# Kernel tuning notes

Measured on AMD Instinct MI355X. Metric: run time of the kernel, lower is better.

## Reference

```python
import jax, jax.numpy as jnp
import numpy as np

EPSILON = 0.15
N_ITERS = 20

def _l2_normalize(x, eps=1e-12):
    n = jnp.linalg.norm(x, axis=-1, keepdims=True)
    return x / jnp.maximum(n, eps)

def setup_inputs() -> dict:
    key = jax.random.key(0)
    k1, k2, k3 = jax.random.split(key, 3)
    B, Ta, Tv, D = 16, 2048, 1024, 512
    return {
        "audio": jax.random.normal(k1, (B, Ta, D), dtype=jnp.float32),
        "video": jax.random.normal(k2, (B, Tv, D), dtype=jnp.float32),
        "quality": jax.random.uniform(k3, (B, Tv), dtype=jnp.float32),
        "lambda_time": jnp.float32(0.5),
        "lambda_qual": jnp.float32(5.0),
    }

def reference(audio, video, quality, lambda_time, lambda_qual):
    B, Ta, D = audio.shape
    Tv = video.shape[1]
    # --- cost matrix ---
    a = _l2_normalize(audio)
    v = _l2_normalize(video)
    sim = jnp.einsum('bad,bvd->bav', a, v)  # [B,Ta,Tv]
    i = jnp.arange(Ta, dtype=jnp.float32)[:, None]
    j = jnp.arange(Tv, dtype=jnp.float32)[None, :]
    time_dist = jnp.abs(i / Ta - j / Tv)  # [Ta,Tv]
    cost = (1.0 - sim) + lambda_time * time_dist[None] \
           + lambda_qual * (1.0 - quality)[:, None, :]
    # --- log-space Sinkhorn (fixed n_iters) ---
    K = -cost / EPSILON
    u0 = jnp.zeros((B, Ta), dtype=cost.dtype)
    v0 = jnp.zeros((B, Tv), dtype=cost.dtype)
    def body(_, uv):
        u, vv = uv
        u = -jax.scipy.special.logsumexp(K + vv[:, None, :], axis=2)
        vv = -jax.scipy.special.logsumexp(K + u[:, :, None], axis=1)
        return (u, vv)
    u, vv = jax.lax.fori_loop(0, N_ITERS, body, (u0, v0))
    transport = jnp.exp(K + u[:, :, None] + vv[:, None, :])
    transport = transport / (jnp.sum(transport, axis=-1, keepdims=True) + 1e-8)
    return transport
```

## Files before the change

kernel.cpp:

```cpp
#include <hip/hip_runtime.h>
#include <hip/hip_fp16.h>

#define B_  16
#define TA  2048
#define TV  1024
#define DD  512
#define NIT 20

static constexpr float EPSI  = 0.15f;
static constexpr float LOG2E = 1.4426950408889634f;

using f32x4 = __attribute__((ext_vector_type(4))) float;
using half8 = __attribute__((ext_vector_type(8))) _Float16;
using half4 = __attribute__((ext_vector_type(4))) _Float16;

__device__ inline float wave_sum(float x) {
  #pragma unroll
  for (int m = 32; m; m >>= 1) x += __shfl_xor(x, m, 64);
  return x;
}

__global__ __launch_bounds__(256) void norms_k(const float* __restrict__ audio,
                                               const float* __restrict__ video,
                                               float* __restrict__ inv_na,
                                               float* __restrict__ inv_nv) {
  int wid  = (blockIdx.x * blockDim.x + threadIdx.x) >> 6;
  int lane = threadIdx.x & 63;
  const float* src;
  float* dst;
  if (wid < B_ * TA) { src = audio + (size_t)wid * DD; dst = inv_na + wid; }
  else               { src = video + (size_t)(wid - B_ * TA) * DD; dst = inv_nv + (wid - B_ * TA); }
  const float4* s4 = (const float4*)src;
  float ss = 0.f;
  #pragma unroll
  for (int i = 0; i < 2; i++) {
    float4 v = s4[lane + i * 64];
    ss += v.x * v.x + v.y * v.y + v.z * v.z + v.w * v.w;
  }
  ss = wave_sum(ss);
  if (lane == 0) *dst = 1.0f / fmaxf(sqrtf(ss), 1e-12f);
}

__global__ void vinit_k(const float* __restrict__ quality,
                        const float* __restrict__ lam_q,
                        float* __restrict__ Vp) {
  int i = blockIdx.x * blockDim.x + threadIdx.x;
  float c1 = LOG2E / EPSI;
  Vp[i] = -c1 * (*lam_q) * (1.0f - quality[i]);
}

#define BM 128
#define BN 128
#define BK 64
#define LDH 72

template<bool F16>
__global__ __launch_bounds__(256) void cost_k(const float* __restrict__ audio,
                                              const float* __restrict__ video,
                                              const float* __restrict__ inv_na,
                                              const float* __restrict__ inv_nv,
                                              const float* __restrict__ lam_t,
                                              float* __restrict__ Kb,
                                              _Float16* __restrict__ Kh) {
  __shared__ _Float16 As[BM * LDH];
  __shared__ _Float16 Bs[BN * LDH];
  int b  = blockIdx.z;
  int a0 = blockIdx.x * BM;
  int j0 = blockIdx.y * BN;
  int tid  = threadIdx.x;
  int lane = tid & 63;
  int wid  = tid >> 6;
  int wm = wid >> 1, wn = wid & 1;

  const float* Ab = audio + (size_t)b * TA * DD;
  const float* Vb = video + (size_t)b * TV * DD;

  f32x4 acc[4][4];
  #pragma unroll
  for (int i = 0; i < 4; i++)
    #pragma unroll
    for (int j = 0; j < 4; j++)
      #pragma unroll
      for (int r = 0; r < 4; r++) acc[i][j][r] = 0.f;

  int frow = tid >> 4;
  int fcol = (tid & 15) * 4;
  int l16 = lane & 15, lq = lane >> 4;

  for (int kb = 0; kb < DD; kb += BK) {
    __syncthreads();
    #pragma unroll
    for (int s = 0; s < 8; s++) {
      int r = frow + s * 16;
      float4 v = *(const float4*)&Ab[(size_t)(a0 + r) * DD + kb + fcol];
      float sc = inv_na[b * TA + a0 + r];
      half4 h = { (_Float16)(v.x * sc), (_Float16)(v.y * sc),
                  (_Float16)(v.z * sc), (_Float16)(v.w * sc) };
      *(half4*)&As[r * LDH + fcol] = h;
    }
    #pragma unroll
    for (int s = 0; s < 8; s++) {
      int r = frow + s * 16;
      float4 v = *(const float4*)&Vb[(size_t)(j0 + r) * DD + kb + fcol];
      float sc = inv_nv[b * TV + j0 + r];
      half4 h = { (_Float16)(v.x * sc), (_Float16)(v.y * sc),
                  (_Float16)(v.z * sc), (_Float16)(v.w * sc) };
      *(half4*)&Bs[r * LDH + fcol] = h;
    }
    __syncthreads();
    #pragma unroll
    for (int ks = 0; ks < 2; ks++) {
      half8 af[4], bf[4];
      #pragma unroll
      for (int mf = 0; mf < 4; mf++)
        af[mf] = *(const half8*)&As[(wm * 64 + mf * 16 + l16) * LDH + ks * 32 + lq * 8];
      #pragma unroll
      for (int nf = 0; nf < 4; nf++)
        bf[nf] = *(const half8*)&Bs[(wn * 64 + nf * 16 + l16) * LDH + ks * 32 + lq * 8];
      #pragma unroll
      for (int mf = 0; mf < 4; mf++)
        #pragma unroll
        for (int nf = 0; nf < 4; nf++)
          acc[mf][nf] = __builtin_amdgcn_mfma_f32_16x16x32_f16(af[mf], bf[nf], acc[mf][nf], 0, 0, 0);
    }
  }

  float lt = *lam_t;
  float c1 = LOG2E / EPSI;
  #pragma unroll
  for (int mf = 0; mf < 4; mf++)
    #pragma unroll
    for (int nf = 0; nf < 4; nf++)
      #pragma unroll
      for (int r = 0; r < 4; r++) {
        int a = a0 + wm * 64 + mf * 16 + lq * 4 + r;
        int j = j0 + wn * 64 + nf * 16 + l16;
        float sim = acc[mf][nf][r];
        float td = fabsf((float)a * (1.0f / TA) - (float)j * (1.0f / TV));
        float val = c1 * (sim - 1.0f - lt * td);
        size_t o = ((size_t)b * TA + a) * TV + j;
        if constexpr (F16) Kh[o] = (_Float16)val;
        else               Kb[o] = val;
      }
}

__global__ __launch_bounds__(512) void iter16_k(const _Float16* __restrict__ Kh,
                                                const float* __restrict__ Vp,
                                                float* __restrict__ pc) {
  __shared__ float lc[8][1024];
  int tid = threadIdx.x, lane = tid & 63, wid = tid >> 6;
  int row0 = (blockIdx.x * 8 + wid) * 8;
  int b = row0 >> 11;
  const float* vp = Vp + b * TV + lane * 8;
  float vpl[16];
  *(float4*)&vpl[0]  = *(const float4*)&vp[0];
  *(float4*)&vpl[4]  = *(const float4*)&vp[4];
  *(float4*)&vpl[8]  = *(const float4*)&vp[512];
  *(float4*)&vpl[12] = *(const float4*)&vp[516];
  float C[16];
  #pragma unroll
  for (int i = 0; i < 16; i++) C[i] = 0.f;

  #pragma unroll 2
  for (int r = 0; r < 8; r++) {
    const _Float16* row = Kh + (size_t)(row0 + r) * TV + lane * 8;
    half8 h0 = *(const half8*)&row[0];
    half8 h1 = *(const half8*)&row[512];
    float e[16];
    float s = 0.f;
    #pragma unroll
    for (int i = 0; i < 8; i++) { e[i] = exp2f((float)h0[i] + vpl[i]); s += e[i]; }
    #pragma unroll
    for (int i = 0; i < 8; i++) { e[8 + i] = exp2f((float)h1[i] + vpl[8 + i]); s += e[8 + i]; }
    s = wave_sum(s);
    float w = 1.0f / s;
    #pragma unroll
    for (int i = 0; i < 16; i++) C[i] = fmaf(e[i], w, C[i]);
  }

  *(float4*)&lc[wid][lane * 8]       = make_float4(C[0], C[1], C[2], C[3]);
  *(float4*)&lc[wid][lane * 8 + 4]   = make_float4(C[4], C[5], C[6], C[7]);
  *(float4*)&lc[wid][512 + lane * 8]     = make_float4(C[8], C[9], C[10], C[11]);
  *(float4*)&lc[wid][512 + lane * 8 + 4] = make_float4(C[12], C[13], C[14], C[15]);
  __syncthreads();
  #pragma unroll
  for (int k = 0; k < 2; k++) {
    int col = tid + k * 512;
    float S = 0.f;
    #pragma unroll
    for (int w = 0; w < 8; w++) S += lc[w][col];
    pc[(size_t)blockIdx.x * 1024 + col] = S;
  }
}

__global__ __launch_bounds__(512) void iter32_k(const float* __restrict__ Kb,
                                                const float* __restrict__ Vp,
                                                float* __restrict__ pc) {
  __shared__ float lc[8][1024];
  int tid = threadIdx.x, lane = tid & 63, wid = tid >> 6;
  int row0 = (blockIdx.x * 8 + wid) * 8;
  int b = row0 >> 11;
  const float* vp = Vp + b * TV;
  float vpl[16];
  #pragma unroll
  for (int q = 0; q < 4; q++)
    *(float4*)&vpl[q * 4] = *(const float4*)&vp[q * 256 + lane * 4];
  float C[16];
  #pragma unroll
  for (int i = 0; i < 16; i++) C[i] = 0.f;

  #pragma unroll 2
  for (int r = 0; r < 8; r++) {
    const float* row = Kb + (size_t)(row0 + r) * TV;
    float e[16];
    float s = 0.f;
    #pragma unroll
    for (int q = 0; q < 4; q++) {
      float4 kv = *(const float4*)&row[q * 256 + lane * 4];
      e[q*4+0] = exp2f(kv.x + vpl[q*4+0]);
      e[q*4+1] = exp2f(kv.y + vpl[q*4+1]);
      e[q*4+2] = exp2f(kv.z + vpl[q*4+2]);
      e[q*4+3] = exp2f(kv.w + vpl[q*4+3]);
      s += e[q*4+0] + e[q*4+1] + e[q*4+2] + e[q*4+3];
    }
    s = wave_sum(s);
    float w = 1.0f / s;
    #pragma unroll
    for (int i = 0; i < 16; i++) C[i] = fmaf(e[i], w, C[i]);
  }

  #pragma unroll
  for (int q = 0; q < 4; q++)
    *(float4*)&lc[wid][q * 256 + lane * 4] =
        make_float4(C[q*4+0], C[q*4+1], C[q*4+2], C[q*4+3]);
  __syncthreads();
  #pragma unroll
  for (int k = 0; k < 2; k++) {
    int col = tid + k * 512;
    float S = 0.f;
    #pragma unroll
    for (int w = 0; w < 8; w++) S += lc[w][col];
    pc[(size_t)blockIdx.x * 1024 + col] = S;
  }
}

__global__ void vcomb_k(const float* __restrict__ pc, float* __restrict__ Vp) {
  int i = blockIdx.x * blockDim.x + threadIdx.x;
  int b = i >> 10, j = i & 1023;
  const float* p = pc + (size_t)(b * 32) * 1024 + j;
  float S = 0.f;
  #pragma unroll
  for (int c = 0; c < 32; c++) S += p[c * 1024];
  Vp[i] -= log2f(S);
}

__global__ __launch_bounds__(256) void final16_k(const _Float16* __restrict__ Kh,
                                                 const float* __restrict__ Vp,
                                                 float* __restrict__ out) {
  int gw   = (blockIdx.x * blockDim.x + threadIdx.x) >> 6;
  int lane = threadIdx.x & 63;
  int b = gw >> 11;
  const float* vp = Vp + b * TV + lane * 8;
  float vpl[16];
  *(float4*)&vpl[0]  = *(const float4*)&vp[0];
  *(float4*)&vpl[4]  = *(const float4*)&vp[4];
  *(float4*)&vpl[8]  = *(const float4*)&vp[512];
  *(float4*)&vpl[12] = *(const float4*)&vp[516];
  const _Float16* row = Kh + (size_t)gw * TV + lane * 8;
  half8 h0 = *(const half8*)&row[0];
  half8 h1 = *(const half8*)&row[512];
  float e[16];
  float s = 0.f;
  #pragma unroll
  for (int i = 0; i < 8; i++) { e[i] = exp2f((float)h0[i] + vpl[i]); s += e[i]; }
  #pragma unroll
  for (int i = 0; i < 8; i++) { e[8 + i] = exp2f((float)h1[i] + vpl[8 + i]); s += e[8 + i]; }
  s = wave_sum(s);
  float inv = 1.0f / s;
  float* o = out + (size_t)gw * TV + lane * 8;
  *(float4*)&o[0]   = make_float4(e[0] * inv, e[1] * inv, e[2] * inv, e[3] * inv);
  *(float4*)&o[4]   = make_float4(e[4] * inv, e[5] * inv, e[6] * inv, e[7] * inv);
  *(float4*)&o[512] = make_float4(e[8] * inv, e[9] * inv, e[10] * inv, e[11] * inv);
  *(float4*)&o[516] = make_float4(e[12] * inv, e[13] * inv, e[14] * inv, e[15] * inv);
}

__global__ __launch_bounds__(256) void final32_k(float* __restrict__ Kb,
                                                 const float* __restrict__ Vp) {
  int gw   = (blockIdx.x * blockDim.x + threadIdx.x) >> 6;
  int lane = threadIdx.x & 63;
  int b = gw >> 11;
  const float* vp = Vp + b * TV;
  float* row = Kb + (size_t)gw * TV;
  float e[16];
  float s = 0.f;
  #pragma unroll
  for (int q = 0; q < 4; q++) {
    float4 kv = *(const float4*)&row[q * 256 + lane * 4];
    float4 vv = *(const float4*)&vp[q * 256 + lane * 4];
    e[q*4+0] = exp2f(kv.x + vv.x); e[q*4+1] = exp2f(kv.y + vv.y);
    e[q*4+2] = exp2f(kv.z + vv.z); e[q*4+3] = exp2f(kv.w + vv.w);
    s += e[q*4+0] + e[q*4+1] + e[q*4+2] + e[q*4+3];
  }
  s = wave_sum(s);
  float inv = 1.0f / s;
  #pragma unroll
  for (int q = 0; q < 4; q++)
    *(float4*)&row[q * 256 + lane * 4] =
        make_float4(e[q*4+0] * inv, e[q*4+1] * inv, e[q*4+2] * inv, e[q*4+3] * inv);
}

extern "C" void kernel_launch(void* const* d_in, const int* in_sizes, int n_in,
                              void* d_out, int out_size, void* d_ws, size_t ws_size,
                              hipStream_t stream) {
  const float* audio   = (const float*)d_in[0];
  const float* video   = (const float*)d_in[1];
  const float* quality = (const float*)d_in[2];
  const float* lam_t   = (const float*)d_in[3];
  const float* lam_q   = (const float*)d_in[4];

  float* out = (float*)d_out;
  float* ws  = (float*)d_ws;
  float* inv_na = ws;
  float* inv_nv = ws + 32768;
  float* Vp     = ws + 49152;
  float* pc     = ws + 65536;
  _Float16* Kh  = (_Float16*)(ws + 589824);

  size_t need_f16 = 589824ull * 4 + (size_t)B_ * TA * TV * 2;

  norms_k<<<12288, 256, 0, stream>>>(audio, video, inv_na, inv_nv);
  vinit_k<<<64, 256, 0, stream>>>(quality, lam_q, Vp);

  if (ws_size >= need_f16) {
    cost_k<true><<<dim3(16, 8, 16), 256, 0, stream>>>(audio, video, inv_na, inv_nv,
                                                      lam_t, nullptr, Kh);
    for (int it = 0; it < NIT; it++) {
      iter16_k<<<512, 512, 0, stream>>>(Kh, Vp, pc);
      vcomb_k<<<64, 256, 0, stream>>>(pc, Vp);
    }
    final16_k<<<8192, 256, 0, stream>>>(Kh, Vp, out);
  } else {
    float* Kb = out;
    cost_k<false><<<dim3(16, 8, 16), 256, 0, stream>>>(audio, video, inv_na, inv_nv,
                                                       lam_t, Kb, nullptr);
    for (int it = 0; it < NIT; it++) {
      iter32_k<<<512, 512, 0, stream>>>(Kb, Vp, pc);
      vcomb_k<<<64, 256, 0, stream>>>(pc, Vp);
    }
    final32_k<<<8192, 256, 0, stream>>>(Kb, Vp);
  }
}
```

Baseline: 486.1 us.

## Fuse Sinkhorn dual update into row pass, pre-normalize inputs to fp16

Adds a new path, used when the workspace is large enough. It first converts normalized audio and video to fp16 in the norms pass, so the GEMM loads half-precision tiles directly and uses a grouped block order. Each Sinkhorn step now reduces the previous step's per-block column partials and applies the log2 update at its own start, which removes the separate vcomb launch. Partials and the V vectors are double-buffered, and the final normalization is folded into the last step. This costs more workspace, redundant 32-way partial reductions in every block, and an extra fp16 copy of the inputs.

```diff
diff --git a/kernel.cpp b/kernel.cpp
--- a/kernel.cpp
+++ b/kernel.cpp
@@ -18,6 +18,38 @@
   #pragma unroll
   for (int m = 32; m; m >>= 1) x += __shfl_xor(x, m, 64);
   return x;
+}
+
+__device__ inline int swz(int c) { return c ^ (((c >> 5) & 7) << 2); }
+
+__global__ __launch_bounds__(256) void norms2_k(const float* __restrict__ audio,
+                                                const float* __restrict__ video,
+                                                _Float16* __restrict__ af16,
+                                                _Float16* __restrict__ vf16,
+                                                float* __restrict__ inv_na,
+                                                float* __restrict__ inv_nv) {
+  int wid  = (blockIdx.x * blockDim.x + threadIdx.x) >> 6;
+  int lane = threadIdx.x & 63;
+  const float* src; _Float16* dst; float* ndst;
+  if (wid < B_ * TA) {
+    src = audio + (size_t)wid * DD; dst = af16 + (size_t)wid * DD; ndst = inv_na + wid;
+  } else {
+    int w2 = wid - B_ * TA;
+    src = video + (size_t)w2 * DD; dst = vf16 + (size_t)w2 * DD; ndst = inv_nv + w2;
+  }
+  float4 v0 = ((const float4*)src)[lane];
+  float4 v1 = ((const float4*)src)[lane + 64];
+  float ss = v0.x*v0.x + v0.y*v0.y + v0.z*v0.z + v0.w*v0.w
+           + v1.x*v1.x + v1.y*v1.y + v1.z*v1.z + v1.w*v1.w;
+  ss = wave_sum(ss);
+  float sc = 1.0f / fmaxf(sqrtf(ss), 1e-12f);
+  if (lane == 0) *ndst = sc;
+  half4 h0 = { (_Float16)(v0.x * sc), (_Float16)(v0.y * sc),
+               (_Float16)(v0.z * sc), (_Float16)(v0.w * sc) };
+  half4 h1 = { (_Float16)(v1.x * sc), (_Float16)(v1.y * sc),
+               (_Float16)(v1.z * sc), (_Float16)(v1.w * sc) };
+  ((half4*)dst)[lane]      = h0;
+  ((half4*)dst)[lane + 64] = h1;
 }
 
 __global__ __launch_bounds__(256) void norms_k(const float* __restrict__ audio,
@@ -26,8 +58,7 @@
                                                float* __restrict__ inv_nv) {
   int wid  = (blockIdx.x * blockDim.x + threadIdx.x) >> 6;
   int lane = threadIdx.x & 63;
-  const float* src;
-  float* dst;
+  const float* src; float* dst;
   if (wid < B_ * TA) { src = audio + (size_t)wid * DD; dst = inv_na + wid; }
   else               { src = video + (size_t)(wid - B_ * TA) * DD; dst = inv_nv + (wid - B_ * TA); }
   const float4* s4 = (const float4*)src;
@@ -53,6 +84,193 @@
 #define BN 128
 #define BK 64
 #define LDH 72
+
+__global__ __launch_bounds__(256) void cost2_k(const _Float16* __restrict__ af16,
+                                               const _Float16* __restrict__ vf16,
+                                               const float* __restrict__ lam_t,
+                                               _Float16* __restrict__ Kh) {
+  __shared__ _Float16 As[BM * LDH];
+  __shared__ _Float16 Bs[BN * LDH];
+  int lin = blockIdx.x;
+  int sw  = (lin & 7) * 256 + (lin >> 3);
+  int b   = sw >> 7;
+  int rem = sw & 127;
+  int j0  = (rem >> 4) * BN;
+  int a0  = (rem & 15) * BM;
+  int tid  = threadIdx.x;
+  int lane = tid & 63;
+  int wid  = tid >> 6;
+  int wm = wid >> 1, wn = wid & 1;
+
+  const _Float16* Ab = af16 + (size_t)b * TA * DD;
+  const _Float16* Vb = vf16 + (size_t)b * TV * DD;
+
+  f32x4 acc[4][4];
+  #pragma unroll
+  for (int i = 0; i < 4; i++)
+    #pragma unroll
+    for (int j = 0; j < 4; j++)
+      #pragma unroll
+      for (int r = 0; r < 4; r++) acc[i][j][r] = 0.f;
+
+  int srow = tid >> 3;
+  int sc8  = (tid & 7) * 8;
+  int l16 = lane & 15, lq = lane >> 4;
+
+  for (int kb = 0; kb < DD; kb += BK) {
+    __syncthreads();
+    #pragma unroll
+    for (int s = 0; s < 4; s++) {
+      int r = srow + s * 32;
+      *(half8*)&As[r * LDH + sc8] = *(const half8*)&Ab[(size_t)(a0 + r) * DD + kb + sc8];
+      *(half8*)&Bs[r * LDH + sc8] = *(const half8*)&Vb[(size_t)(j0 + r) * DD + kb + sc8];
+    }
+    __syncthreads();
+    #pragma unroll
+    for (int ks = 0; ks < 2; ks++) {
+      half8 af[4], bf[4];
+      #pragma unroll
+      for (int mf = 0; mf < 4; mf++)
+        af[mf] = *(const half8*)&As[(wm * 64 + mf * 16 + l16) * LDH + ks * 32 + lq * 8];
+      #pragma unroll
+      for (int nf = 0; nf < 4; nf++)
+        bf[nf] = *(const half8*)&Bs[(wn * 64 + nf * 16 + l16) * LDH + ks * 32 + lq * 8];
+      #pragma unroll
+      for (int mf = 0; mf < 4; mf++)
+        #pragma unroll
+        for (int nf = 0; nf < 4; nf++)
+          acc[mf][nf] = __builtin_amdgcn_mfma_f32_16x16x32_f16(af[mf], bf[nf], acc[mf][nf], 0, 0, 0);
+    }
+  }
+
+  float lt = *lam_t;
+  float c1 = LOG2E / EPSI;
+  #pragma unroll
+  for (int mf = 0; mf < 4; mf++)
+    #pragma unroll
+    for (int nf = 0; nf < 4; nf++)
+      #pragma unroll
+      for (int r = 0; r < 4; r++) {
+        int a = a0 + wm * 64 + mf * 16 + lq * 4 + r;
+        int j = j0 + wn * 64 + nf * 16 + l16;
+        float sim = acc[mf][nf][r];
+        float td = fabsf((float)a * (1.0f / TA) - (float)j * (1.0f / TV));
+        Kh[((size_t)b * TA + a) * TV + j] = (_Float16)(c1 * (sim - 1.0f - lt * td));
+      }
+}
+
+template<int MODE>
+__global__ __launch_bounds__(512) void step_k(const _Float16* __restrict__ Kh,
+                                              const float* __restrict__ Vp_in,
+                                              float* __restrict__ Vp_out,
+                                              const float* __restrict__ pc_in,
+                                              float* __restrict__ pc_out,
+                                              float* __restrict__ out) {
+  __shared__ float lc[8][1024];
+  __shared__ float vbuf[1024];
+  const int tid = threadIdx.x, lane = tid & 63, wid = tid >> 6;
+  const int bid  = blockIdx.x;
+  const int row0 = bid * 64 + wid * 8;
+  const int b    = bid >> 5;
+
+  if (MODE == 0) {
+    #pragma unroll
+    for (int k = 0; k < 2; k++) {
+      int col = tid + k * 512;
+      vbuf[swz(col)] = Vp_in[b * TV + col];
+    }
+  } else {
+    #pragma unroll
+    for (int k = 0; k < 2; k++) {
+      int col = tid + k * 512;
+      const float* p = pc_in + ((size_t)b * 32) * 1024 + col;
+      float S = 0.f;
+      #pragma unroll
+      for (int c = 0; c < 32; c++) S += p[c * 1024];
+      float nv = Vp_in[b * TV + col] - log2f(S);
+      vbuf[swz(col)] = nv;
+      if (MODE == 1 && (bid & 31) == 0) Vp_out[b * TV + col] = nv;
+    }
+  }
+  __syncthreads();
+
+  float vpl[16];
+  *(f32x4*)&vpl[0]  = *(const f32x4*)&vbuf[swz(lane * 8)];
+  *(f32x4*)&vpl[4]  = *(const f32x4*)&vbuf[swz(lane * 8 + 4)];
+  *(f32x4*)&vpl[8]  = *(const f32x4*)&vbuf[swz(512 + lane * 8)];
+  *(f32x4*)&vpl[12] = *(const f32x4*)&vbuf[swz(512 + lane * 8 + 4)];
+
+  float C[16];
+  #pragma unroll
+  for (int i = 0; i < 16; i++) C[i] = 0.f;
+
+  #pragma unroll
+  for (int pr = 0; pr < 4; pr++) {
+    const _Float16* rp0 = Kh + (size_t)(row0 + pr * 2) * TV + lane * 8;
+    const _Float16* rp1 = Kh + (size_t)(row0 + pr * 2 + 1) * TV + lane * 8;
+    half8 a0 = *(const half8*)&rp0[0];
+    half8 a1 = *(const half8*)&rp0[512];
+    half8 b0 = *(const half8*)&rp1[0];
+    half8 b1 = *(const half8*)&rp1[512];
+    float e0[16], e1[16];
+    float s0 = 0.f, s1 = 0.f;
+    #pragma unroll
+    for (int i = 0; i < 8; i++) {
+      e0[i] = exp2f((float)a0[i] + vpl[i]);     s0 += e0[i];
+      e1[i] = exp2f((float)b0[i] + vpl[i]);     s1 += e1[i];
+    }
+    #pragma unroll
+    for (int i = 0; i < 8; i++) {
+      e0[8+i] = exp2f((float)a1[i] + vpl[8+i]); s0 += e0[8+i];
+      e1[8+i] = exp2f((float)b1[i] + vpl[8+i]); s1 += e1[8+i];
+    }
+    #pragma unroll
+    for (int m = 32; m; m >>= 1) {
+      s0 += __shfl_xor(s0, m, 64);
+      s1 += __shfl_xor(s1, m, 64);
+    }
+    float w0 = 1.0f / s0, w1 = 1.0f / s1;
+    if (MODE == 2) {
+      float* o0 = out + (size_t)(row0 + pr * 2) * TV + lane * 8;
+      float* o1 = out + (size_t)(row0 + pr * 2 + 1) * TV + lane * 8;
+      f32x4 t;
+      t = (f32x4){e0[0]*w0, e0[1]*w0, e0[2]*w0, e0[3]*w0};     *(f32x4*)&o0[0]   = t;
+      t = (f32x4){e0[4]*w0, e0[5]*w0, e0[6]*w0, e0[7]*w0};     *(f32x4*)&o0[4]   = t;
+      t = (f32x4){e0[8]*w0, e0[9]*w0, e0[10]*w0, e0[11]*w0};   *(f32x4*)&o0[512] = t;
+      t = (f32x4){e0[12]*w0, e0[13]*w0, e0[14]*w0, e0[15]*w0}; *(f32x4*)&o0[516] = t;
+      t = (f32x4){e1[0]*w1, e1[1]*w1, e1[2]*w1, e1[3]*w1};     *(f32x4*)&o1[0]   = t;
+      t = (f32x4){e1[4]*w1, e1[5]*w1, e1[6]*w1, e1[7]*w1};     *(f32x4*)&o1[4]   = t;
+      t = (f32x4){e1[8]*w1, e1[9]*w1, e1[10]*w1, e1[11]*w1};   *(f32x4*)&o1[512] = t;
+      t = (f32x4){e1[12]*w1, e1[13]*w1, e1[14]*w1, e1[15]*w1}; *(f32x4*)&o1[516] = t;
+    } else {
+      #pragma unroll
+      for (int i = 0; i < 16; i++)
+        C[i] = fmaf(e0[i], w0, fmaf(e1[i], w1, C[i]));
+    }
+  }
+
+  if (MODE != 2) {
+    #pragma unroll
+    for (int q = 0; q < 4; q++) {
+      *(f32x4*)&lc[wid][swz(lane * 8 + ((q & 1) ? 4 : 0) + ((q >> 1) ? 512 : 0))] =
+          *(f32x4*)&C[q * 4 - ((q == 1) ? 0 : 0)];
+    }
+    *(f32x4*)&lc[wid][swz(lane * 8)]           = *(f32x4*)&C[0];
+    *(f32x4*)&lc[wid][swz(lane * 8 + 4)]       = *(f32x4*)&C[4];
+    *(f32x4*)&lc[wid][swz(512 + lane * 8)]     = *(f32x4*)&C[8];
+    *(f32x4*)&lc[wid][swz(512 + lane * 8 + 4)] = *(f32x4*)&C[12];
+    __syncthreads();
+    #pragma unroll
+    for (int k = 0; k < 2; k++) {
+      int col = tid + k * 512;
+      int sc_ = swz(col);
+      float S = 0.f;
+      #pragma unroll
+      for (int w = 0; w < 8; w++) S += lc[w][sc_];
+      pc_out[(size_t)bid * 1024 + col] = S;
+    }
+  }
+}
 
 template<bool F16>
 __global__ __launch_bounds__(256) void cost_k(const float* __restrict__ audio,
@@ -71,10 +289,8 @@
   int lane = tid & 63;
   int wid  = tid >> 6;
   int wm = wid >> 1, wn = wid & 1;
-
   const float* Ab = audio + (size_t)b * TA * DD;
   const float* Vb = video + (size_t)b * TV * DD;
-
   f32x4 acc[4][4];
   #pragma unroll
   for (int i = 0; i < 4; i++)
@@ -82,11 +298,9 @@
     for (int j = 0; j < 4; j++)
       #pragma unroll
       for (int r = 0; r < 4; r++) acc[i][j][r] = 0.f;
-
   int frow = tid >> 4;
   int fcol = (tid & 15) * 4;
   int l16 = lane & 15, lq = lane >> 4;
-
   for (int kb = 0; kb < DD; kb += BK) {
     __syncthreads();
     #pragma unroll
@@ -124,7 +338,6 @@
           acc[mf][nf] = __builtin_amdgcn_mfma_f32_16x16x32_f16(af[mf], bf[nf], acc[mf][nf], 0, 0, 0);
     }
   }
-
   float lt = *lam_t;
   float c1 = LOG2E / EPSI;
   #pragma unroll
@@ -160,7 +373,6 @@
   float C[16];
   #pragma unroll
   for (int i = 0; i < 16; i++) C[i] = 0.f;
-
   #pragma unroll 2
   for (int r = 0; r < 8; r++) {
     const _Float16* row = Kh + (size_t)(row0 + r) * TV + lane * 8;
@@ -177,9 +389,8 @@
     #pragma unroll
     for (int i = 0; i < 16; i++) C[i] = fmaf(e[i], w, C[i]);
   }
-
-  *(float4*)&lc[wid][lane * 8]       = make_float4(C[0], C[1], C[2], C[3]);
-  *(float4*)&lc[wid][lane * 8 + 4]   = make_float4(C[4], C[5], C[6], C[7]);
+  *(float4*)&lc[wid][lane * 8]           = make_float4(C[0], C[1], C[2], C[3]);
+  *(float4*)&lc[wid][lane * 8 + 4]       = make_float4(C[4], C[5], C[6], C[7]);
   *(float4*)&lc[wid][512 + lane * 8]     = make_float4(C[8], C[9], C[10], C[11]);
   *(float4*)&lc[wid][512 + lane * 8 + 4] = make_float4(C[12], C[13], C[14], C[15]);
   __syncthreads();
@@ -208,7 +419,6 @@
   float C[16];
   #pragma unroll
   for (int i = 0; i < 16; i++) C[i] = 0.f;
-
   #pragma unroll 2
   for (int r = 0; r < 8; r++) {
     const float* row = Kb + (size_t)(row0 + r) * TV;
@@ -228,7 +438,6 @@
     #pragma unroll
     for (int i = 0; i < 16; i++) C[i] = fmaf(e[i], w, C[i]);
   }
-
   #pragma unroll
   for (int q = 0; q < 4; q++)
     *(float4*)&lc[wid][q * 256 + lane * 4] =
@@ -322,31 +531,54 @@
   float* ws  = (float*)d_ws;
   float* inv_na = ws;
   float* inv_nv = ws + 32768;
-  float* Vp     = ws + 49152;
-  float* pc     = ws + 65536;
-  _Float16* Kh  = (_Float16*)(ws + 589824);
-
-  size_t need_f16 = 589824ull * 4 + (size_t)B_ * TA * TV * 2;
-
-  norms_k<<<12288, 256, 0, stream>>>(audio, video, inv_na, inv_nv);
-  vinit_k<<<64, 256, 0, stream>>>(quality, lam_q, Vp);
-
-  if (ws_size >= need_f16) {
+  float* VpX    = ws + 49152;
+  float* VpY    = ws + 65536;
+  float* pcA    = ws + 81920;
+  float* pcB    = ws + 606208;
+  _Float16* af16 = (_Float16*)(ws + 1130496);
+  _Float16* vf16 = (_Float16*)(ws + 9519104);
+  _Float16* KhF  = (_Float16*)(ws + 13713408);
+  size_t need_full = 30490624ull * 4;
+
+  float* VpM    = ws + 49152;
+  float* pcM    = ws + 65536;
+  _Float16* KhM = (_Float16*)(ws + 589824);
+  size_t need_mid = (589824ull + 16777216ull) * 4;
+
+  if (ws_size >= need_full) {
+    norms2_k<<<12288, 256, 0, stream>>>(audio, video, af16, vf16, inv_na, inv_nv);
+    vinit_k<<<64, 256, 0, stream>>>(quality, lam_q, VpX);
+    cost2_k<<<2048, 256, 0, stream>>>(af16, vf16, lam_t, KhF);
+
+    step_k<0><<<512, 512, 0, stream>>>(KhF, VpX, nullptr, nullptr, pcA, nullptr);
+    float* vin = VpX; float* vout = VpY;
+    float* pin = pcA; float* pout = pcB;
+    for (int t = 2; t <= NIT; t++) {
+      step_k<1><<<512, 512, 0, stream>>>(KhF, vin, vout, pin, pout, nullptr);
+      float* tmp = vin; vin = vout; vout = tmp;
+      tmp = pin; pin = pout; pout = tmp;
+    }
+    step_k<2><<<512, 512, 0, stream>>>(KhF, vin, nullptr, pin, nullptr, out);
+  } else if (ws_size >= need_mid) {
+    norms_k<<<12288, 256, 0, stream>>>(audio, video, inv_na, inv_nv);
+    vinit_k<<<64, 256, 0, stream>>>(quality, lam_q, VpM);
     cost_k<true><<<dim3(16, 8, 16), 256, 0, stream>>>(audio, video, inv_na, inv_nv,
-                                                      lam_t, nullptr, Kh);
+                                                      lam_t, nullptr, KhM);
     for (int it = 0; it < NIT; it++) {
-      iter16_k<<<512, 512, 0, stream>>>(Kh, Vp, pc);
-      vcomb_k<<<64, 256, 0, stream>>>(pc, Vp);
-    }
-    final16_k<<<8192, 256, 0, stream>>>(Kh, Vp, out);
+      iter16_k<<<512, 512, 0, stream>>>(KhM, VpM, pcM);
+      vcomb_k<<<64, 256, 0, stream>>>(pcM, VpM);
+    }
+    final16_k<<<8192, 256, 0, stream>>>(KhM, VpM, out);
   } else {
+    norms_k<<<12288, 256, 0, stream>>>(audio, video, inv_na, inv_nv);
+    vinit_k<<<64, 256, 0, stream>>>(quality, lam_q, VpM);
     float* Kb = out;
     cost_k<false><<<dim3(16, 8, 16), 256, 0, stream>>>(audio, video, inv_na, inv_nv,
                                                        lam_t, Kb, nullptr);
     for (int it = 0; it < NIT; it++) {
-      iter32_k<<<512, 512, 0, stream>>>(Kb, Vp, pc);
-      vcomb_k<<<64, 256, 0, stream>>>(pc, Vp);
-    }
-    final32_k<<<8192, 256, 0, stream>>>(Kb, Vp);
-  }
-}
+      iter32_k<<<512, 512, 0, stream>>>(Kb, VpM, pcM);
+      vcomb_k<<<64, 256, 0, stream>>>(pcM, VpM);
+    }
+    final32_k<<<8192, 256, 0, stream>>>(Kb, VpM);
+  }
+}
```

After: 611.1 us. 25.7% more time.
